# Optimization experiments

Hardware: AMD Instinct MI355X
Metric: run time of the kernel (lower is better)

## Reference

```python
import jax, jax.numpy as jnp
import numpy as np

B, T, D, L, K = 4, 2048, 2048, 2048, 4  # batch, seq, width, lru_width, conv temporal width


def setup_inputs() -> dict:
    key = jax.random.key(0)
    ks = jax.random.split(key, 12)
    s = 0.02
    f32 = jnp.float32
    return {
        "x": jax.random.normal(ks[0], (B, T, D), f32),
        "w_y": jax.random.normal(ks[1], (D, L), f32) * s,
        "b_y": jnp.zeros((L,), f32),
        "w_x": jax.random.normal(ks[2], (D, L), f32) * s,
        "b_x": jnp.zeros((L,), f32),
        "conv_w": jax.random.normal(ks[3], (K, L), f32) * s,
        "conv_b": jnp.zeros((L,), f32),
        "a_param": jax.random.uniform(ks[4], (L,), f32, 0.5, 4.0),
        "w_ig": jax.random.normal(ks[5], (L, L), f32) * s,
        "b_ig": jnp.zeros((L,), f32),
        "w_ag": jax.random.normal(ks[6], (L, L), f32) * s,
        "b_ag": jnp.zeros((L,), f32),
        "w_out": jax.random.normal(ks[7], (L, D), f32) * s,
        "b_out": jnp.zeros((D,), f32),
    }


def reference(x, w_y, b_y, w_x, b_x, conv_w, conv_b, a_param,
              w_ig, b_ig, w_ag, b_ag, w_out, b_out):
    # x: [B, T, D] (batch_first=True)
    Tn = x.shape[1]
    # gate branch: GELU(linear_y(x))
    y = jax.nn.gelu(jnp.einsum('btd,dl->btl', x, w_y) + b_y, approximate=False)
    # recurrent branch: linear_x -> causal depthwise conv1d (width K)
    xb = jnp.einsum('btd,dl->btl', x, w_x) + b_x
    xp = jnp.pad(xb, ((0, 0), (K - 1, 0), (0, 0)))  # zero left pad (fresh cache)
    conv = conv_b
    for k in range(K):  # y_t = b + sum_k w[k] * x_{t-(K-1-k)}
        conv = conv + conv_w[k] * xp[:, k:k + Tn]
    # RG-LRU
    gate_x = jax.nn.sigmoid(jnp.einsum('btl,lm->btm', conv, w_ig) + b_ig)
    gate_a = jax.nn.sigmoid(jnp.einsum('btl,lm->btm', conv, w_ag) + b_ag)
    log_a = -8.0 * gate_a * jax.nn.softplus(a_param)  # [B,T,L]
    a = jnp.exp(log_a)
    mult = jnp.sqrt(1.0 - jnp.exp(2.0 * log_a))
    reset = (jnp.arange(Tn) == 0)[None, :, None]  # reset at sequence start
    a = jnp.where(reset, 0.0, a)
    mult = jnp.where(reset, 1.0, mult)
    nx = gate_x * conv * mult
    # linear diagonal scan h_t = a_t * h_{t-1} + nx_t
    def step(h, inp):
        a_t, x_t = inp
        h = a_t * h + x_t
        return h, h
    h0 = jnp.zeros((x.shape[0], a.shape[-1]), x.dtype)
    hn, hs = jax.lax.scan(step, h0, (a.transpose(1, 0, 2), nx.transpose(1, 0, 2)))
    h_seq = hs.transpose(1, 0, 2)  # [B,T,L]
    out = jnp.einsum('btl,ld->btd', h_seq * y, w_out) + b_out
    return out, hn
```

## Files before the change

kernel.cpp:

```cpp
#include <hip/hip_runtime.h>
#include <math.h>

#define B_ 4
#define T_ 2048
#define D_ 2048
#define L_ 2048
#define KW 4
#define M_ (B_*T_)

typedef unsigned short u16;
typedef unsigned short u16x8 __attribute__((ext_vector_type(8)));
typedef __bf16 bf16x8 __attribute__((ext_vector_type(8)));
typedef float f32x4 __attribute__((ext_vector_type(4)));

__device__ __forceinline__ u16 f2bf(float f) {
    unsigned u = __float_as_uint(f);
    u += 0x7fffu + ((u >> 16) & 1u);
    return (u16)(u >> 16);
}
__device__ __forceinline__ float bf2f(u16 h) {
    return __uint_as_float(((unsigned)h) << 16);
}
__device__ __forceinline__ float gelu_exact(float v) {
    return 0.5f * v * (1.0f + erff(v * 0.70710678118654752440f));
}
__device__ __forceinline__ float sigmoidf_(float v) {
    return 1.0f / (1.0f + __expf(-v));
}
__device__ __forceinline__ void gload16(const void* g, void* l) {
    __builtin_amdgcn_global_load_lds(
        (const __attribute__((address_space(1))) void*)g,
        (__attribute__((address_space(3))) void*)l,
        16, 0, 0);
}
__device__ __forceinline__ void bar() {
    __builtin_amdgcn_s_barrier();
}

__global__ __launch_bounds__(256)
void castx_kernel(const float* __restrict__ in, u16* __restrict__ out)
{
    const int i = blockIdx.x * 256 + threadIdx.x;
    float4 v = ((const float4*)in)[i];
    ushort4 o;
    o.x = f2bf(v.x); o.y = f2bf(v.y); o.z = f2bf(v.z); o.w = f2bf(v.w);
    ((ushort4*)out)[i] = o;
}

__global__ __launch_bounds__(256)
void transcast_kernel(const float* __restrict__ in, u16* __restrict__ out,
                      int Kd, int Nd)
{
    __shared__ float tile[32][33];
    const int bx = blockIdx.x;
    const int by = blockIdx.y;
    const int tx = threadIdx.x & 31;
    const int ty = threadIdx.x >> 5;
    #pragma unroll
    for (int j = 0; j < 4; ++j) {
        const int r = by*32 + ty + j*8;
        tile[ty + j*8][tx] = in[(size_t)r * Nd + bx*32 + tx];
    }
    __syncthreads();
    #pragma unroll
    for (int j = 0; j < 4; ++j) {
        const int n = bx*32 + ty + j*8;
        out[(size_t)n * Kd + by*32 + tx] = f2bf(tile[tx][ty + j*8]);
    }
}

__device__ __forceinline__ void store_out(float* C, size_t idx, float v) { C[idx] = v; }
__device__ __forceinline__ void store_out(u16*   C, size_t idx, float v) { C[idx] = f2bf(v); }

template<int EPI, typename OutT>
__global__ __launch_bounds__(512, 4)
void mgemm_kernel(const u16* __restrict__ A, const u16* __restrict__ BT,
                  const float* __restrict__ bias, OutT* __restrict__ C,
                  int M, int N, int K)
{
    __shared__ __align__(16) u16 lds[36864];
    u16* ldsB = lds + 24576;

    const int tid  = threadIdx.x;
    const int wave = tid >> 6;
    const int lane = tid & 63;

    const int nbx = N >> 7;
    const int nwg = nbx * (M >> 8);
    const int bid = blockIdx.x;
    const int li  = (bid & 7) * (nwg >> 3) + (bid >> 3);
    const int bm  = (li / nbx) * 256;
    const int bn  = (li % nbx) * 128;

    const int wr = wave >> 1;
    const int wn = wave & 1;
    const int lr = lane & 15;
    const int q  = lane >> 4;

    const int grow  = lane >> 2;
    const int gslot = (lane & 3) ^ ((lane >> 3) & 3);
    const u16* gA0 = A  + (size_t)(bm + wave*16     + grow) * K + gslot*8;
    const u16* gA1 = A  + (size_t)(bm + (wave+8)*16 + grow) * K + gslot*8;
    const u16* gB0 = BT + (size_t)(bn + wave*16     + grow) * K + gslot*8;
    const int dA0 = wave*512     + lane*8;
    const int dA1 = (wave+8)*512 + lane*8;
    const int dB0 = wave*512     + lane*8;

    auto STAGE = [&](int g) {
        const int s = g % 3;
        const size_t kg = (size_t)g << 5;
        u16* a = lds  + s*8192;
        u16* b = ldsB + s*4096;
        gload16(gA0 + kg, &a[dA0]);
        gload16(gA1 + kg, &a[dA1]);
        gload16(gB0 + kg, &b[dB0]);
    };

    const int ksw = (q ^ ((lr >> 1) & 3)) * 8;

    f32x4 acc[4][4] = {};

    STAGE(0); STAGE(1);
    asm volatile("s_waitcnt vmcnt(3)" ::: "memory");
    bar();

    const int NT = K >> 5;
    for (int g = 0; g < NT; ++g) {
        const int s = g % 3;
        const u16* Ab = lds  + s*8192;
        const u16* Bb = ldsB + s*4096;

        bf16x8 a[4], b[4];
        #pragma unroll
        for (int i = 0; i < 4; ++i)
            a[i] = *(const bf16x8*)&Ab[(wr*64 + i*16 + lr)*32 + ksw];
        #pragma unroll
        for (int j = 0; j < 4; ++j)
            b[j] = *(const bf16x8*)&Bb[(wn*64 + j*16 + lr)*32 + ksw];

        if (g + 2 < NT) STAGE(g + 2);

        __builtin_amdgcn_s_setprio(1);
        #pragma unroll
        for (int i = 0; i < 4; ++i)
            #pragma unroll
            for (int j = 0; j < 4; ++j)
                acc[i][j] = __builtin_amdgcn_mfma_f32_16x16x32_bf16(a[i], b[j], acc[i][j], 0, 0, 0);
        __builtin_amdgcn_s_setprio(0);

        if (g + 2 < NT)      { asm volatile("s_waitcnt vmcnt(3)" ::: "memory"); }
        else if (g + 1 < NT) { asm volatile("s_waitcnt vmcnt(0)" ::: "memory"); }
        bar();
    }

    const int orow = (lane >> 4) * 4;
    float bv[4];
    #pragma unroll
    for (int nj = 0; nj < 4; ++nj) bv[nj] = bias[bn + wn*64 + nj*16 + lr];
    #pragma unroll
    for (int mi = 0; mi < 4; ++mi) {
        #pragma unroll
        for (int r = 0; r < 4; ++r) {
            const int row = bm + wr*64 + mi*16 + orow + r;
            const size_t rb = (size_t)row * N + bn + wn*64 + lr;
            #pragma unroll
            for (int nj = 0; nj < 4; ++nj) {
                float v = acc[mi][nj][r] + bv[nj];
                if (EPI == 1)      v = gelu_exact(v);
                else if (EPI == 2) v = sigmoidf_(v);
                store_out(C, rb + nj*16, v);
            }
        }
    }
}

__global__ __launch_bounds__(256)
void conv_kernel(const u16* __restrict__ xb, const float* __restrict__ cw,
                 const float* __restrict__ cb, u16* __restrict__ out)
{
    const int idx = blockIdx.x * 256 + threadIdx.x;
    const int NL8 = L_ / 8;
    const int l = (idx % NL8) * 8;
    const int bt = idx / NL8;
    const int t = bt & (T_ - 1);
    float acc[8];
    #pragma unroll
    for (int j = 0; j < 8; ++j) acc[j] = cb[l + j];
    #pragma unroll
    for (int k = 0; k < KW; ++k) {
        const int ts = t - (KW-1) + k;
        if (ts >= 0) {
            u16x8 xv = *(const u16x8*)(xb + ((size_t)(bt - (KW-1-k))) * L_ + l);
            #pragma unroll
            for (int j = 0; j < 8; ++j)
                acc[j] = fmaf(cw[k*L_ + l + j], bf2f(xv[j]), acc[j]);
        }
    }
    u16x8 o;
    #pragma unroll
    for (int j = 0; j < 8; ++j) o[j] = f2bf(acc[j]);
    *(u16x8*)(out + (size_t)bt * L_ + l) = o;
}

__global__ __launch_bounds__(256)
void rglru_kernel(const u16* __restrict__ conv, u16* __restrict__ gxa,
                  u16* __restrict__ ganx, const float* __restrict__ ap)
{
    const int idx = blockIdx.x * 256 + threadIdx.x;
    const int NL8 = L_ / 8;
    const int l = (idx % NL8) * 8;
    const int bt = idx / NL8;
    const int t = bt & (T_ - 1);
    const size_t off = (size_t)bt * L_ + l;
    u16x8 gx = *(u16x8*)(gxa + off);
    u16x8 ga = *(u16x8*)(ganx + off);
    u16x8 cv = *(const u16x8*)(conv + off);
    u16x8 av, nxv;
    #pragma unroll
    for (int j = 0; j < 8; ++j) {
        float p  = ap[l + j];
        float sp = log1pf(expf(p));
        float la = -8.0f * bf2f(ga[j]) * sp;
        float a  = expf(la);
        float mult = sqrtf(fmaxf(0.f, 1.0f - a*a));
        if (t == 0) { a = 0.f; mult = 1.f; }
        av[j]  = f2bf(a);
        nxv[j] = f2bf(bf2f(gx[j]) * bf2f(cv[j]) * mult);
    }
    *(u16x8*)(gxa + off)  = av;
    *(u16x8*)(ganx + off) = nxv;
}

#define CHUNKS 32
#define CLEN (T_ / CHUNKS)

__global__ __launch_bounds__(256)
void scan1_kernel(const u16* __restrict__ Ab, const u16* __restrict__ Xb,
                  float* __restrict__ Pb, float* __restrict__ Sb)
{
    const int l = blockIdx.x * 256 + threadIdx.x;
    const int c = blockIdx.y;
    const int b = blockIdx.z;
    size_t base = ((size_t)b * T_ + (size_t)c * CLEN) * L_ + l;
    float h = 0.f, P = 1.f;
    #pragma unroll 4
    for (int t = 0; t < CLEN; ++t) {
        float a = bf2f(Ab[base + (size_t)t * L_]);
        float x = bf2f(Xb[base + (size_t)t * L_]);
        h = fmaf(a, h, x);
        P *= a;
    }
    const size_t o = ((size_t)b * CHUNKS + c) * L_ + l;
    Pb[o] = P;
    Sb[o] = h;
}

__global__ __launch_bounds__(256)
void scan2_kernel(const float* __restrict__ Pb, const float* __restrict__ Sb,
                  float* __restrict__ Hin, float* __restrict__ hn)
{
    const int idx = blockIdx.x * 256 + threadIdx.x;
    const int l = idx & (L_ - 1);
    const int b = idx >> 11;
    float h = 0.f;
    for (int c = 0; c < CHUNKS; ++c) {
        const size_t o = ((size_t)b * CHUNKS + c) * L_ + l;
        Hin[o] = h;
        h = fmaf(Pb[o], h, Sb[o]);
    }
    hn[(size_t)b * L_ + l] = h;
}

__global__ __launch_bounds__(256)
void scan3_kernel(const u16* __restrict__ Ab, const u16* __restrict__ Xb,
                  const float* __restrict__ Hin, const u16* __restrict__ Yb,
                  u16* __restrict__ Zb)
{
    const int l = blockIdx.x * 256 + threadIdx.x;
    const int c = blockIdx.y;
    const int b = blockIdx.z;
    float h = Hin[((size_t)b * CHUNKS + c) * L_ + l];
    size_t base = ((size_t)b * T_ + (size_t)c * CLEN) * L_ + l;
    #pragma unroll 4
    for (int t = 0; t < CLEN; ++t) {
        const size_t o = base + (size_t)t * L_;
        h = fmaf(bf2f(Ab[o]), h, bf2f(Xb[o]));
        Zb[o] = f2bf(h * bf2f(Yb[o]));
    }
}

extern "C" void kernel_launch(void* const* d_in, const int* in_sizes, int n_in,
                              void* d_out, int out_size, void* d_ws, size_t ws_size,
                              hipStream_t stream)
{
    const float* x     = (const float*)d_in[0];
    const float* w_y   = (const float*)d_in[1];
    const float* b_y   = (const float*)d_in[2];
    const float* w_x   = (const float*)d_in[3];
    const float* b_x   = (const float*)d_in[4];
    const float* cw    = (const float*)d_in[5];
    const float* cb    = (const float*)d_in[6];
    const float* ap    = (const float*)d_in[7];
    const float* w_ig  = (const float*)d_in[8];
    const float* b_ig  = (const float*)d_in[9];
    const float* w_ag  = (const float*)d_in[10];
    const float* b_ag  = (const float*)d_in[11];
    const float* w_out = (const float*)d_in[12];
    const float* b_out = (const float*)d_in[13];

    float* out = (float*)d_out;
    float* hn  = out + (size_t)M_ * D_;

    const size_t MB = 1u << 20;
    char* w = (char*)d_ws;
    u16*  xbf   = (u16*)(w + 0);
    u16*  wigb  = (u16*)(w + 0);
    u16*  wagb  = (u16*)(w + 8*MB);
    u16*  zb    = (u16*)(w + 0);
    u16*  ybf   = (u16*)(w + 32*MB);
    u16*  xbbf  = (u16*)(w + 64*MB);
    u16*  woutb = (u16*)(w + 64*MB);
    float* Pb   = (float*)(w + 72*MB);
    float* Sb   = (float*)(w + 73*MB);
    float* Hin  = (float*)(w + 74*MB);
    u16*  wyb   = (u16*)(w + 96*MB);
    u16*  wxb   = (u16*)(w + 104*MB);
    u16*  convb = (u16*)(w + 96*MB);
    u16*  gx    = (u16*)(w + 128*MB);
    u16*  ga    = (u16*)(w + 160*MB);

    const dim3 blk(256);
    const dim3 blkG(512);
    const dim3 gG((L_/128) * (M_/256));
    const dim3 gT(2048/32, 2048/32);
    const int  gE8 = (M_ * L_ / 8) / 256;
    const dim3 gScan(L_/256, CHUNKS, B_);

    hipLaunchKernelGGL(castx_kernel, dim3((M_*D_/4)/256), blk, 0, stream, x, xbf);
    hipLaunchKernelGGL(transcast_kernel, gT, blk, 0, stream, w_y, wyb, D_, L_);
    hipLaunchKernelGGL(transcast_kernel, gT, blk, 0, stream, w_x, wxb, D_, L_);
    hipLaunchKernelGGL((mgemm_kernel<1, u16>), gG, blkG, 0, stream, xbf, wyb, b_y, ybf, M_, L_, D_);
    hipLaunchKernelGGL((mgemm_kernel<0, u16>), gG, blkG, 0, stream, xbf, wxb, b_x, xbbf, M_, L_, D_);
    hipLaunchKernelGGL(transcast_kernel, gT, blk, 0, stream, w_ig, wigb, L_, L_);
    hipLaunchKernelGGL(transcast_kernel, gT, blk, 0, stream, w_ag, wagb, L_, L_);
    hipLaunchKernelGGL(conv_kernel, dim3(gE8), blk, 0, stream, xbbf, cw, cb, convb);
    hipLaunchKernelGGL(transcast_kernel, gT, blk, 0, stream, w_out, woutb, L_, D_);
    hipLaunchKernelGGL((mgemm_kernel<2, u16>), gG, blkG, 0, stream, convb, wigb, b_ig, gx, M_, L_, L_);
    hipLaunchKernelGGL((mgemm_kernel<2, u16>), gG, blkG, 0, stream, convb, wagb, b_ag, ga, M_, L_, L_);
    hipLaunchKernelGGL(rglru_kernel, dim3(gE8), blk, 0, stream, convb, gx, ga, ap);
    hipLaunchKernelGGL(scan1_kernel, gScan, blk, 0, stream, gx, ga, Pb, Sb);
    hipLaunchKernelGGL(scan2_kernel, dim3(B_*L_/256), blk, 0, stream, Pb, Sb, Hin, hn);
    hipLaunchKernelGGL(scan3_kernel, gScan, blk, 0, stream, gx, ga, Hin, ybf, zb);
    hipLaunchKernelGGL((mgemm_kernel<0, float>), gG, blkG, 0, stream, zb, woutb, b_out, out, M_, D_, L_);
}
```

Before: 579.0 us.

## Fuse paired input GEMMs into dual-B kernel and fold RG-LRU epilogue

```diff
diff --git a/kernel.cpp b/kernel.cpp
--- a/kernel.cpp
+++ b/kernel.cpp
@@ -66,6 +66,141 @@
     for (int j = 0; j < 4; ++j) {
         const int n = bx*32 + ty + j*8;
         out[(size_t)n * Kd + by*32 + tx] = f2bf(tile[tx][ty + j*8]);
+    }
+}
+
+template<int MODE>
+__global__ __launch_bounds__(256)
+void dgemm_kernel(const u16* __restrict__ A, const u16* __restrict__ B1T,
+                  const u16* __restrict__ B2T,
+                  const float* __restrict__ bias1, const float* __restrict__ bias2,
+                  u16* __restrict__ C1, u16* __restrict__ C2,
+                  const u16* __restrict__ convp, const float* __restrict__ ap,
+                  int M, int N, int K)
+{
+    __shared__ __align__(16) u16 lds[36864];
+    u16* ldsB1 = lds + 12288;
+    u16* ldsB2 = lds + 24576;
+
+    const int tid  = threadIdx.x;
+    const int wave = tid >> 6;
+    const int lane = tid & 63;
+
+    const int nbx = N >> 7;
+    const int nwg = nbx * (M >> 7);
+    const int bid = blockIdx.x;
+    const int li  = (bid & 7) * (nwg >> 3) + (bid >> 3);
+    const int bm  = (li / nbx) * 128;
+    const int bn  = (li % nbx) * 128;
+
+    const int wr = wave >> 1;
+    const int wn = wave & 1;
+    const int lr = lane & 15;
+    const int q  = lane >> 4;
+
+    const int grow  = lane >> 2;
+    const int gslot = (lane & 3) ^ ((lane >> 3) & 3);
+    const u16* gA0  = A   + (size_t)(bm + wave*16     + grow) * K + gslot*8;
+    const u16* gA1  = A   + (size_t)(bm + (wave+4)*16 + grow) * K + gslot*8;
+    const u16* gB10 = B1T + (size_t)(bn + wave*16     + grow) * K + gslot*8;
+    const u16* gB11 = B1T + (size_t)(bn + (wave+4)*16 + grow) * K + gslot*8;
+    const u16* gB20 = B2T + (size_t)(bn + wave*16     + grow) * K + gslot*8;
+    const u16* gB21 = B2T + (size_t)(bn + (wave+4)*16 + grow) * K + gslot*8;
+    const int d0 = wave*512     + lane*8;
+    const int d1 = (wave+4)*512 + lane*8;
+
+    auto STAGE = [&](int g) {
+        const int s = g % 3;
+        const size_t kg = (size_t)g << 5;
+        u16* a  = lds   + s*4096;
+        u16* b1 = ldsB1 + s*4096;
+        u16* b2 = ldsB2 + s*4096;
+        gload16(gA0  + kg, &a [d0]);
+        gload16(gA1  + kg, &a [d1]);
+        gload16(gB10 + kg, &b1[d0]);
+        gload16(gB11 + kg, &b1[d1]);
+        gload16(gB20 + kg, &b2[d0]);
+        gload16(gB21 + kg, &b2[d1]);
+    };
+
+    const int ksw = (q ^ ((lr >> 1) & 3)) * 8;
+
+    f32x4 acc1[4][4] = {};
+    f32x4 acc2[4][4] = {};
+
+    STAGE(0); STAGE(1);
+    asm volatile("s_waitcnt vmcnt(6)" ::: "memory");
+    bar();
+
+    const int NT = K >> 5;
+    for (int g = 0; g < NT; ++g) {
+        const int s = g % 3;
+        const u16* Ab  = lds   + s*4096;
+        const u16* B1b = ldsB1 + s*4096;
+        const u16* B2b = ldsB2 + s*4096;
+
+        bf16x8 a[4], b1[4], b2[4];
+        #pragma unroll
+        for (int i = 0; i < 4; ++i)
+            a[i] = *(const bf16x8*)&Ab[(wr*64 + i*16 + lr)*32 + ksw];
+        #pragma unroll
+        for (int j = 0; j < 4; ++j) {
+            b1[j] = *(const bf16x8*)&B1b[(wn*64 + j*16 + lr)*32 + ksw];
+            b2[j] = *(const bf16x8*)&B2b[(wn*64 + j*16 + lr)*32 + ksw];
+        }
+
+        if (g + 2 < NT) STAGE(g + 2);
+
+        __builtin_amdgcn_s_setprio(1);
+        #pragma unroll
+        for (int i = 0; i < 4; ++i)
+            #pragma unroll
+            for (int j = 0; j < 4; ++j) {
+                acc1[i][j] = __builtin_amdgcn_mfma_f32_16x16x32_bf16(a[i], b1[j], acc1[i][j], 0, 0, 0);
+                acc2[i][j] = __builtin_amdgcn_mfma_f32_16x16x32_bf16(a[i], b2[j], acc2[i][j], 0, 0, 0);
+            }
+        __builtin_amdgcn_s_setprio(0);
+
+        if (g + 2 < NT)      { asm volatile("s_waitcnt vmcnt(6)" ::: "memory"); }
+        else if (g + 1 < NT) { asm volatile("s_waitcnt vmcnt(0)" ::: "memory"); }
+        bar();
+    }
+
+    const int orow = (lane >> 4) * 4;
+    float bv1[4], bv2[4], spv[4];
+    #pragma unroll
+    for (int nj = 0; nj < 4; ++nj) {
+        const int col = bn + wn*64 + nj*16 + lr;
+        bv1[nj] = bias1[col];
+        bv2[nj] = bias2[col];
+        if (MODE == 1) spv[nj] = log1pf(expf(ap[col]));
+    }
+    #pragma unroll
+    for (int mi = 0; mi < 4; ++mi) {
+        #pragma unroll
+        for (int r = 0; r < 4; ++r) {
+            const int row = bm + wr*64 + mi*16 + orow + r;
+            const size_t rb = (size_t)row * N + bn + wn*64 + lr;
+            const int t = row & (T_ - 1);
+            #pragma unroll
+            for (int nj = 0; nj < 4; ++nj) {
+                const float v1 = acc1[mi][nj][r] + bv1[nj];
+                const float v2 = acc2[mi][nj][r] + bv2[nj];
+                if (MODE == 0) {
+                    C1[rb + nj*16] = f2bf(gelu_exact(v1));
+                    C2[rb + nj*16] = f2bf(v2);
+                } else {
+                    const float g1 = sigmoidf_(v1);
+                    const float g2 = sigmoidf_(v2);
+                    float a    = expf(-8.0f * g2 * spv[nj]);
+                    float mult = sqrtf(fmaxf(0.f, 1.0f - a*a));
+                    if (t == 0) { a = 0.f; mult = 1.f; }
+                    const float cv = bf2f(convp[rb + nj*16]);
+                    C1[rb + nj*16] = f2bf(a);
+                    C2[rb + nj*16] = f2bf(g1 * cv * mult);
+                }
+            }
+        }
     }
 }
 
@@ -166,8 +301,6 @@
             #pragma unroll
             for (int nj = 0; nj < 4; ++nj) {
                 float v = acc[mi][nj][r] + bv[nj];
-                if (EPI == 1)      v = gelu_exact(v);
-                else if (EPI == 2) v = sigmoidf_(v);
                 store_out(C, rb + nj*16, v);
             }
         }
@@ -200,35 +333,6 @@
     #pragma unroll
     for (int j = 0; j < 8; ++j) o[j] = f2bf(acc[j]);
     *(u16x8*)(out + (size_t)bt * L_ + l) = o;
-}
-
-__global__ __launch_bounds__(256)
-void rglru_kernel(const u16* __restrict__ conv, u16* __restrict__ gxa,
-                  u16* __restrict__ ganx, const float* __restrict__ ap)
-{
-    const int idx = blockIdx.x * 256 + threadIdx.x;
-    const int NL8 = L_ / 8;
-    const int l = (idx % NL8) * 8;
-    const int bt = idx / NL8;
-    const int t = bt & (T_ - 1);
-    const size_t off = (size_t)bt * L_ + l;
-    u16x8 gx = *(u16x8*)(gxa + off);
-    u16x8 ga = *(u16x8*)(ganx + off);
-    u16x8 cv = *(const u16x8*)(conv + off);
-    u16x8 av, nxv;
-    #pragma unroll
-    for (int j = 0; j < 8; ++j) {
-        float p  = ap[l + j];
-        float sp = log1pf(expf(p));
-        float la = -8.0f * bf2f(ga[j]) * sp;
-        float a  = expf(la);
-        float mult = sqrtf(fmaxf(0.f, 1.0f - a*a));
-        if (t == 0) { a = 0.f; mult = 1.f; }
-        av[j]  = f2bf(a);
-        nxv[j] = f2bf(bf2f(gx[j]) * bf2f(cv[j]) * mult);
-    }
-    *(u16x8*)(gxa + off)  = av;
-    *(u16x8*)(ganx + off) = nxv;
 }
 
 #define CHUNKS 32
@@ -331,6 +435,7 @@
 
     const dim3 blk(256);
     const dim3 blkG(512);
+    const dim3 gD((L_/128) * (M_/128));
     const dim3 gG((L_/128) * (M_/256));
     const dim3 gT(2048/32, 2048/32);
     const int  gE8 = (M_ * L_ / 8) / 256;
@@ -339,15 +444,15 @@
     hipLaunchKernelGGL(castx_kernel, dim3((M_*D_/4)/256), blk, 0, stream, x, xbf);
     hipLaunchKernelGGL(transcast_kernel, gT, blk, 0, stream, w_y, wyb, D_, L_);
     hipLaunchKernelGGL(transcast_kernel, gT, blk, 0, stream, w_x, wxb, D_, L_);
-    hipLaunchKernelGGL((mgemm_kernel<1, u16>), gG, blkG, 0, stream, xbf, wyb, b_y, ybf, M_, L_, D_);
-    hipLaunchKernelGGL((mgemm_kernel<0, u16>), gG, blkG, 0, stream, xbf, wxb, b_x, xbbf, M_, L_, D_);
+    hipLaunchKernelGGL((dgemm_kernel<0>), gD, blk, 0, stream,
+                       xbf, wyb, wxb, b_y, b_x, ybf, xbbf,
+                       (const u16*)nullptr, (const float*)nullptr, M_, L_, D_);
     hipLaunchKernelGGL(transcast_kernel, gT, blk, 0, stream, w_ig, wigb, L_, L_);
     hipLaunchKernelGGL(transcast_kernel, gT, blk, 0, stream, w_ag, wagb, L_, L_);
     hipLaunchKernelGGL(conv_kernel, dim3(gE8), blk, 0, stream, xbbf, cw, cb, convb);
     hipLaunchKernelGGL(transcast_kernel, gT, blk, 0, stream, w_out, woutb, L_, D_);
-    hipLaunchKernelGGL((mgemm_kernel<2, u16>), gG, blkG, 0, stream, convb, wigb, b_ig, gx, M_, L_, L_);
-    hipLaunchKernelGGL((mgemm_kernel<2, u16>), gG, blkG, 0, stream, convb, wagb, b_ag, ga, M_, L_, L_);
-    hipLaunchKernelGGL(rglru_kernel, dim3(gE8), blk, 0, stream, convb, gx, ga, ap);
+    hipLaunchKernelGGL((dgemm_kernel<1>), gD, blk, 0, stream,
+                       convb, wigb, wagb, b_ig, b_ag, gx, ga, convb, ap, M_, L_, L_);
     hipLaunchKernelGGL(scan1_kernel, gScan, blk, 0, stream, gx, ga, Pb, Sb);
     hipLaunchKernelGGL(scan2_kernel, dim3(B_*L_/256), blk, 0, stream, Pb, Sb, Hin, hn);
     hipLaunchKernelGGL(scan3_kernel, gScan, blk, 0, stream, gx, ga, Hin, ybf, zb);
```

Measured after the change: 585.1 us. Within noise of the previous version (+1.1%).
